# Kernel optimization log

Hardware: AMD Instinct MI355X
Metric: run time of the kernel (lower is better)

Reference implementation:

```python
import jax, jax.numpy as jnp
import numpy as np

B, L, H, I, K, G = 2, 4096, 1024, 2048, 4, 8  # batch, seq, hidden, intermediate, kernel, conv groups
EPS = 1e-5


def setup_inputs() -> dict:
    key = jax.random.key(0)
    ks = jax.random.split(key, 8)
    s = 0.02
    return {
        "hidden_states": jax.random.normal(ks[0], (B, L, H), jnp.float32),
        "in_proj_w": jax.random.normal(ks[1], (2 * I, H), jnp.float32) * s,  # Linear(H -> 2I), no bias
        "conv_w": jax.random.normal(ks[2], (I, I // G, K), jnp.float32) * s,  # grouped Conv1d weight [O, I/G, K]
        "conv_b": jax.random.normal(ks[3], (I,), jnp.float32) * s,
        "ln_g": jnp.ones((I,), jnp.float32),
        "ln_b": jnp.zeros((I,), jnp.float32),
        "fc_w": jax.random.normal(ks[4], (H, I), jnp.float32) * s,   # MLP c_fc: I -> H
        "fc_b": jnp.zeros((H,), jnp.float32),
        "cproj_w": jax.random.normal(ks[5], (I, H), jnp.float32) * s,  # MLP c_proj: H -> I
        "cproj_b": jnp.zeros((I,), jnp.float32),
        "out_w": jax.random.normal(ks[6], (H, I), jnp.float32) * s,  # out_proj: I -> H, no bias
    }


def _layernorm(x, g, b):
    m = x.mean(-1, keepdims=True)
    v = jnp.var(x, axis=-1, keepdims=True)
    return (x - m) * jax.lax.rsqrt(v + EPS) * g + b


def reference(hidden_states, in_proj_w, conv_w, conv_b, ln_g, ln_b, fc_w, fc_b, cproj_w, cproj_b, out_w):
    # in_proj then chunk into hidden / gate (torch chunks along channel dim after transpose)
    p = hidden_states @ in_proj_w.T              # [B, L, 2I]
    h, gate = p[..., :I], p[..., I:]             # [B, L, I] each
    gate = jax.nn.silu(gate)
    # causal grouped conv1d: ConstantPad1d((K-1, 0)) + Conv1d(groups=G)
    hc = jnp.transpose(h, (0, 2, 1))             # [B, I, L]
    conv = jax.lax.conv_general_dilated(
        hc, conv_w, window_strides=(1,), padding=[(K - 1, 0)],
        feature_group_count=G, dimension_numbers=("NCH", "OIH", "NCH"))
    conv = conv + conv_b[None, :, None]          # [B, I, L]
    h = jnp.transpose(conv, (0, 2, 1)) * gate    # gated mixing, [B, L, I]
    residual = h
    hn = _layernorm(h, ln_g, ln_b)
    # MLP (dropout is identity at inference): I -> H -> silu -> I
    m = jax.nn.silu(hn @ fc_w.T + fc_b) @ cproj_w.T + cproj_b
    h = m + residual
    return h @ out_w.T                           # [B, L, H]
```

## Files before the change

kernel.cpp:

```cpp
#include <hip/hip_runtime.h>
#include <stdint.h>


#define TOKENS 8192
#define HDIM   1024
#define IDIM   2048
#define PADL   4099

typedef __bf16 bf16_t;
typedef __bf16 bf16x8 __attribute__((ext_vector_type(8)));
typedef __bf16 bf16x4 __attribute__((ext_vector_type(4)));
typedef float  f32x4  __attribute__((ext_vector_type(4)));

__device__ __forceinline__ float silu_f(float v) { return v / (1.f + __expf(-v)); }

__global__ __launch_bounds__(256) void cvt_f32_bf16(const float* __restrict__ in,
                                                    bf16_t* __restrict__ out, int n4) {
  int i = blockIdx.x * 256 + threadIdx.x;
  if (i < n4) {
    float4 v = reinterpret_cast<const float4*>(in)[i];
    bf16x4 o = {(bf16_t)v.x, (bf16_t)v.y, (bf16_t)v.z, (bf16_t)v.w};
    reinterpret_cast<bf16x4*>(out)[i] = o;
  }
}

__global__ __launch_bounds__(256) void cvt_weights(
    const float* __restrict__ ipf, const float* __restrict__ fcf,
    const float* __restrict__ cpf, const float* __restrict__ outf,
    bf16_t* __restrict__ ipb, bf16_t* __restrict__ fcb,
    bf16_t* __restrict__ cpb, bf16_t* __restrict__ outb) {
  int i = blockIdx.x * 256 + threadIdx.x;
  const float* src; bf16_t* dst; int off;
  if (i < 1048576)      { src = ipf;  dst = ipb;  off = i; }
  else if (i < 1572864) { src = fcf;  dst = fcb;  off = i - 1048576; }
  else if (i < 2097152) { src = cpf;  dst = cpb;  off = i - 1572864; }
  else                  { src = outf; dst = outb; off = i - 2097152; }
  float4 v = reinterpret_cast<const float4*>(src)[off];
  bf16x4 o = {(bf16_t)v.x, (bf16_t)v.y, (bf16_t)v.z, (bf16_t)v.w};
  reinterpret_cast<bf16x4*>(dst)[off] = o;
}

__global__ __launch_bounds__(256) void expand_convw(const float* __restrict__ cw,
                                                    bf16_t* __restrict__ w2) {
  int idx = blockIdx.x * 256 + threadIdx.x;
  int o = idx >> 10, r = idx & 1023, k = r >> 8, ci = r & 255;
  w2[idx] = (bf16_t)cw[(o << 10) + (ci << 2) + k];
}

__global__ __launch_bounds__(256) void zero_pad_rows(bf16_t* __restrict__ hpad) {
  int idx = blockIdx.x * 256 + threadIdx.x;
  if (idx < 2 * 3 * IDIM) {
    int b = idx / (3 * IDIM);
    int r = idx - b * (3 * IDIM);
    hpad[(size_t)b * PADL * IDIM + r] = (bf16_t)0.f;
  }
}

__global__ __launch_bounds__(256) void ln_k(const bf16_t* __restrict__ x,
                                            const float* __restrict__ g,
                                            const float* __restrict__ b,
                                            bf16_t* __restrict__ out) {
  int row = blockIdx.x, tid = threadIdx.x;
  const bf16_t* xr = x + (size_t)row * IDIM;
  bf16x8 v = *reinterpret_cast<const bf16x8*>(xr + tid * 8);
  float f[8], s = 0.f, ss = 0.f;
#pragma unroll
  for (int j = 0; j < 8; ++j) { f[j] = (float)v[j]; s += f[j]; ss += f[j] * f[j]; }
#pragma unroll
  for (int o = 32; o; o >>= 1) { s += __shfl_xor(s, o); ss += __shfl_xor(ss, o); }
  __shared__ float red[2][4];
  int wv = tid >> 6, lane = tid & 63;
  if (lane == 0) { red[0][wv] = s; red[1][wv] = ss; }
  __syncthreads();
  s  = red[0][0] + red[0][1] + red[0][2] + red[0][3];
  ss = red[1][0] + red[1][1] + red[1][2] + red[1][3];
  float mean = s * (1.f / IDIM);
  float var  = ss * (1.f / IDIM) - mean * mean;
  float rstd = rsqrtf(var + 1e-5f);
  bf16x8 o8;
#pragma unroll
  for (int j = 0; j < 8; ++j) {
    int c = tid * 8 + j;
    o8[j] = (bf16_t)((f[j] - mean) * rstd * g[c] + b[c]);
  }
  *reinterpret_cast<bf16x8*>(out + (size_t)row * IDIM + tid * 8) = o8;
}

#define BARR __builtin_amdgcn_s_barrier()

template <int KIND, int N, int K, int BM, int BN, int WM, int WN>
__global__ __launch_bounds__(WM * WN * 64, 2) void gemm_k(
    const bf16_t* __restrict__ A, const bf16_t* __restrict__ W,
    const float* __restrict__ bias, const bf16_t* __restrict__ extra,
    void* __restrict__ outp, bf16_t* __restrict__ hpad_out,
    bf16_t* __restrict__ gate_out) {
  constexpr int NWAVE = WM * WN;
  constexpr int TM = BM / WM, TN = BN / WN;
  constexpr int MR = TM / 16, NR = TN / 16;
  constexpr int NT = K / 64;
  constexpr int NTN = N / BN;
  constexpr int SA = BM / (NWAVE * 8);
  constexpr int SB = BN / (NWAVE * 8);
  __shared__ bf16_t As[2][BM][64];
  __shared__ bf16_t Bs[2][BN][64];
  const int tid = threadIdx.x, lane = tid & 63, wid = tid >> 6;
  const int wr = wid / WN, wc = wid % WN;
  int bid = blockIdx.x;
  { const int cpx = gridDim.x >> 3; bid = (bid & 7) * cpx + (bid >> 3); }
  const int t0 = (bid / NTN) * BM, n0 = (bid % NTN) * BN;

  const int sw16 = (((lane & 7) ^ (lane >> 3)) << 4);

  int cur = 0;

  auto stageA = [&](int j, int tt) {
    const int row = j * NWAVE * 8 + wid * 8 + (lane >> 3);
    char* dst = (char*)&As[tt & 1][0][0] + row * 128 + ((lane & 7) << 4);
    const char* src;
    if constexpr (KIND == 1) {
      const int grow = t0 + row, b = grow >> 12, pos = grow & 4095;
      src = (const char*)A +
            (((size_t)b * PADL + pos + (tt >> 2)) * IDIM + (n0 & ~255) + ((tt & 3) << 6)) * 2 + sw16;
    } else {
      src = (const char*)A + ((size_t)(t0 + row) * K + tt * 64) * 2 + sw16;
    }
    __builtin_amdgcn_global_load_lds((const __attribute__((address_space(1))) void*)src,
                                     (__attribute__((address_space(3))) void*)dst, 16, 0, 0);
  };
  auto stageB = [&](int j, int tt) {
    const int row = j * NWAVE * 8 + wid * 8 + (lane >> 3);
    char* dst = (char*)&Bs[tt & 1][0][0] + row * 128 + ((lane & 7) << 4);
    const char* src = (const char*)W + ((size_t)(n0 + row) * K + tt * 64) * 2 + sw16;
    __builtin_amdgcn_global_load_lds((const __attribute__((address_space(1))) void*)src,
                                     (__attribute__((address_space(3))) void*)dst, 16, 0, 0);
  };
  auto stageAll = [&](int tt) {
#pragma unroll
    for (int j = 0; j < SA; ++j) stageA(j, tt);
#pragma unroll
    for (int j = 0; j < SB; ++j) stageB(j, tt);
  };
  auto readA = [&](int mi, int s) -> bf16x8 {
    const int row = wr * TM + mi * 16 + (lane & 15);
    const int cb = (s * 64 + ((lane >> 4) << 4)) ^ ((lane & 7) << 4);
    return *(const bf16x8*)((const char*)&As[cur][0][0] + row * 128 + cb);
  };
  auto readB = [&](int ni, int s) -> bf16x8 {
    const int row = wc * TN + ni * 16 + (lane & 15);
    const int cb = (s * 64 + ((lane >> 4) << 4)) ^ ((lane & 7) << 4);
    return *(const bf16x8*)((const char*)&Bs[cur][0][0] + row * 128 + cb);
  };

  f32x4 acc[MR][NR] = {};
  bf16x8 aF[MR / 2][2], bF[NR][2];

#define MMA_QUAD(MH, NH)                                                        \
  _Pragma("unroll") for (int mi = 0; mi < MR / 2; ++mi) {                       \
    _Pragma("unroll") for (int ni = 0; ni < NR / 2; ++ni) {                     \
      _Pragma("unroll") for (int s = 0; s < 2; ++s) {                           \
        acc[(MH) * (MR / 2) + mi][(NH) * (NR / 2) + ni] =                       \
            __builtin_amdgcn_mfma_f32_16x16x32_bf16(                            \
                aF[mi][s], bF[(NH) * (NR / 2) + ni][s],                         \
                acc[(MH) * (MR / 2) + mi][(NH) * (NR / 2) + ni], 0, 0, 0);      \
      }                                                                         \
    }                                                                           \
  }

  stageAll(0);
  asm volatile("s_waitcnt vmcnt(0)");
  BARR;

  for (int t = 0; t < NT; ++t) {
    cur = t & 1;
    const bool nx = (t + 1) < NT;
#pragma unroll
    for (int mi = 0; mi < MR / 2; ++mi)
#pragma unroll
      for (int s = 0; s < 2; ++s) aF[mi][s] = readA(mi, s);
#pragma unroll
    for (int ni = 0; ni < NR / 2; ++ni)
#pragma unroll
      for (int s = 0; s < 2; ++s) bF[ni][s] = readB(ni, s);
    if (nx) stageAll(t + 1);
    BARR;
    __builtin_amdgcn_s_setprio(1);
    MMA_QUAD(0, 0);
    __builtin_amdgcn_s_setprio(0);
    BARR;
#pragma unroll
    for (int ni = 0; ni < NR / 2; ++ni)
#pragma unroll
      for (int s = 0; s < 2; ++s) bF[NR / 2 + ni][s] = readB(NR / 2 + ni, s);
    BARR;
    __builtin_amdgcn_s_setprio(1);
    MMA_QUAD(0, 1);
    __builtin_amdgcn_s_setprio(0);
    BARR;
#pragma unroll
    for (int mi = 0; mi < MR / 2; ++mi)
#pragma unroll
      for (int s = 0; s < 2; ++s) aF[mi][s] = readA(MR / 2 + mi, s);
    BARR;
    __builtin_amdgcn_s_setprio(1);
    MMA_QUAD(1, 1);
    __builtin_amdgcn_s_setprio(0);
    BARR;
    __builtin_amdgcn_s_setprio(1);
    MMA_QUAD(1, 0);
    __builtin_amdgcn_s_setprio(0);
    if (nx) asm volatile("s_waitcnt vmcnt(0)");
    BARR;
  }
#undef MMA_QUAD

#pragma unroll
  for (int mi = 0; mi < MR; ++mi) {
#pragma unroll
    for (int ni = 0; ni < NR; ++ni) {
      const int col = n0 + wc * TN + ni * 16 + (lane & 15);
      float bv = 0.f;
      if constexpr (KIND == 1 || KIND == 2 || KIND == 3) bv = bias[col];
#pragma unroll
      for (int r = 0; r < 4; ++r) {
        const int row = t0 + wr * TM + mi * 16 + ((lane >> 4) << 2) + r;
        float v = acc[mi][ni][r];
        if constexpr (KIND == 0) {
          if (n0 < IDIM) {
            int b = row >> 12, pos = row & 4095;
            hpad_out[((size_t)b * PADL + 3 + pos) * IDIM + col] = (bf16_t)v;
          } else {
            gate_out[(size_t)row * IDIM + (col - IDIM)] = (bf16_t)silu_f(v);
          }
        } else if constexpr (KIND == 1) {
          float gt = (float)extra[(size_t)row * IDIM + col];
          ((bf16_t*)outp)[(size_t)row * N + col] = (bf16_t)((v + bv) * gt);
        } else if constexpr (KIND == 2) {
          ((bf16_t*)outp)[(size_t)row * N + col] = (bf16_t)silu_f(v + bv);
        } else if constexpr (KIND == 3) {
          float res = (float)extra[(size_t)row * N + col];
          ((bf16_t*)outp)[(size_t)row * N + col] = (bf16_t)(v + bv + res);
        } else {
          ((float*)outp)[(size_t)row * N + col] = v;
        }
      }
    }
  }
}

extern "C" void kernel_launch(void* const* d_in, const int* in_sizes, int n_in,
                              void* d_out, int out_size, void* d_ws, size_t ws_size,
                              hipStream_t stream) {
  const float* hs       = (const float*)d_in[0];
  const float* in_projw = (const float*)d_in[1];
  const float* conv_w   = (const float*)d_in[2];
  const float* conv_b   = (const float*)d_in[3];
  const float* ln_g     = (const float*)d_in[4];
  const float* ln_b     = (const float*)d_in[5];
  const float* fc_w     = (const float*)d_in[6];
  const float* fc_b     = (const float*)d_in[7];
  const float* cproj_w  = (const float*)d_in[8];
  const float* cproj_b  = (const float*)d_in[9];
  const float* out_w    = (const float*)d_in[10];

  char* ws = (char*)d_ws;
  size_t off = 0;
  auto alloc = [&](size_t bytes) {
    char* p = ws + off;
    off += (bytes + 255) & ~(size_t)255;
    return p;
  };
  bf16_t* hs_b  = (bf16_t*)alloc((size_t)TOKENS * HDIM * 2);
  bf16_t* w_ip  = (bf16_t*)alloc((size_t)2 * IDIM * HDIM * 2);
  bf16_t* w2c   = (bf16_t*)alloc((size_t)IDIM * 1024 * 2);
  bf16_t* w_fc  = (bf16_t*)alloc((size_t)HDIM * IDIM * 2);
  bf16_t* w_cp  = (bf16_t*)alloc((size_t)IDIM * HDIM * 2);
  bf16_t* w_out = (bf16_t*)alloc((size_t)HDIM * IDIM * 2);
  bf16_t* hpad  = (bf16_t*)alloc((size_t)2 * PADL * IDIM * 2);
  bf16_t* gate  = (bf16_t*)alloc((size_t)TOKENS * IDIM * 2);
  bf16_t* xres  = (bf16_t*)alloc((size_t)TOKENS * IDIM * 2);

  bf16_t* t_buf = hs_b;
  bf16_t* hn    = gate;
  bf16_t* h2    = hpad;

  cvt_f32_bf16<<<8192, 256, 0, stream>>>(hs, hs_b, TOKENS * HDIM / 4);
  cvt_weights<<<10240, 256, 0, stream>>>(in_projw, fc_w, cproj_w, out_w,
                                         w_ip, w_fc, w_cp, w_out);
  expand_convw<<<8192, 256, 0, stream>>>(conv_w, w2c);
  zero_pad_rows<<<48, 256, 0, stream>>>(hpad);

  gemm_k<0, 4096, 1024, 256, 256, 2, 4><<<512, 512, 0, stream>>>(
      hs_b, w_ip, nullptr, nullptr, nullptr, hpad, gate);
  gemm_k<1, 2048, 1024, 256, 256, 2, 4><<<256, 512, 0, stream>>>(
      hpad, w2c, conv_b, gate, xres, nullptr, nullptr);
  ln_k<<<TOKENS, 256, 0, stream>>>(xres, ln_g, ln_b, hn);
  gemm_k<2, 1024, 2048, 256, 128, 2, 4><<<256, 512, 0, stream>>>(
      hn, w_fc, fc_b, nullptr, t_buf, nullptr, nullptr);
  gemm_k<3, 2048, 1024, 256, 256, 2, 4><<<256, 512, 0, stream>>>(
      t_buf, w_cp, cproj_b, xres, h2, nullptr, nullptr);
  gemm_k<4, 1024, 2048, 256, 128, 2, 4><<<256, 512, 0, stream>>>(
      h2, w_out, nullptr, nullptr, d_out, nullptr, nullptr);
}
```

Measured before the change: 463.4 us.

## Interleave next-tile LDS staging across MMA quadrants with partial vmcnt waits

```diff
diff --git a/kernel.cpp b/kernel.cpp
--- a/kernel.cpp
+++ b/kernel.cpp
@@ -88,6 +88,13 @@
 
 #define BARR __builtin_amdgcn_s_barrier()
 
+template <int N> __device__ __forceinline__ void vwait() {
+  if constexpr (N == 0) asm volatile("s_waitcnt vmcnt(0)");
+  else if constexpr (N == 2) asm volatile("s_waitcnt vmcnt(2)");
+  else if constexpr (N == 3) asm volatile("s_waitcnt vmcnt(3)");
+  else if constexpr (N == 4) asm volatile("s_waitcnt vmcnt(4)");
+}
+
 template <int KIND, int N, int K, int BM, int BN, int WM, int WN>
 __global__ __launch_bounds__(WM * WN * 64, 2) void gemm_k(
     const bf16_t* __restrict__ A, const bf16_t* __restrict__ W,
@@ -101,6 +108,9 @@
   constexpr int NTN = N / BN;
   constexpr int SA = BM / (NWAVE * 8);
   constexpr int SB = BN / (NWAVE * 8);
+  static_assert(TM / SA == WN * 8, "A stage map");
+  static_assert(TN / SB == WM * 8, "B stage map");
+  static_assert(SA == 4 && (SB == 4 || SB == 2), "ledger assumes SA=4");
   __shared__ bf16_t As[2][BM][64];
   __shared__ bf16_t Bs[2][BN][64];
   const int tid = threadIdx.x, lane = tid & 63, wid = tid >> 6;
@@ -114,7 +124,7 @@
   int cur = 0;
 
   auto stageA = [&](int j, int tt) {
-    const int row = j * NWAVE * 8 + wid * 8 + (lane >> 3);
+    const int row = wr * TM + j * (TM / SA) + (wc << 3) + (lane >> 3);
     char* dst = (char*)&As[tt & 1][0][0] + row * 128 + ((lane & 7) << 4);
     const char* src;
     if constexpr (KIND == 1) {
@@ -128,17 +138,11 @@
                                      (__attribute__((address_space(3))) void*)dst, 16, 0, 0);
   };
   auto stageB = [&](int j, int tt) {
-    const int row = j * NWAVE * 8 + wid * 8 + (lane >> 3);
+    const int row = wc * TN + j * (TN / SB) + (wr << 3) + (lane >> 3);
     char* dst = (char*)&Bs[tt & 1][0][0] + row * 128 + ((lane & 7) << 4);
     const char* src = (const char*)W + ((size_t)(n0 + row) * K + tt * 64) * 2 + sw16;
     __builtin_amdgcn_global_load_lds((const __attribute__((address_space(1))) void*)src,
                                      (__attribute__((address_space(3))) void*)dst, 16, 0, 0);
-  };
-  auto stageAll = [&](int tt) {
-#pragma unroll
-    for (int j = 0; j < SA; ++j) stageA(j, tt);
-#pragma unroll
-    for (int j = 0; j < SB; ++j) stageB(j, tt);
   };
   auto readA = [&](int mi, int s) -> bf16x8 {
     const int row = wr * TM + mi * 16 + (lane & 15);
@@ -166,8 +170,10 @@
     }                                                                           \
   }
 
-  stageAll(0);
-  asm volatile("s_waitcnt vmcnt(0)");
+  stageA(0, 0); stageA(1, 0); stageB(0, 0); stageB(1, 0);
+  if constexpr (SB == 4) { stageB(2, 0); stageB(3, 0); }
+  stageA(2, 0); stageA(3, 0);
+  if constexpr (SB == 4) vwait<4>(); else vwait<3>();
   BARR;
 
   for (int t = 0; t < NT; ++t) {
@@ -181,34 +187,45 @@
     for (int ni = 0; ni < NR / 2; ++ni)
 #pragma unroll
       for (int s = 0; s < 2; ++s) bF[ni][s] = readB(ni, s);
-    if (nx) stageAll(t + 1);
+    if (nx) { stageA(0, t + 1); stageA(1, t + 1); }
     BARR;
     __builtin_amdgcn_s_setprio(1);
     MMA_QUAD(0, 0);
     __builtin_amdgcn_s_setprio(0);
+    if (nx) vwait<4>(); else vwait<2>();
     BARR;
 #pragma unroll
     for (int ni = 0; ni < NR / 2; ++ni)
 #pragma unroll
       for (int s = 0; s < 2; ++s) bF[NR / 2 + ni][s] = readB(NR / 2 + ni, s);
+    if (nx) { stageB(0, t + 1); stageB(1, t + 1); }
     BARR;
     __builtin_amdgcn_s_setprio(1);
     MMA_QUAD(0, 1);
     __builtin_amdgcn_s_setprio(0);
+    if (nx) vwait<4>(); else vwait<0>();
     BARR;
 #pragma unroll
     for (int mi = 0; mi < MR / 2; ++mi)
 #pragma unroll
       for (int s = 0; s < 2; ++s) aF[mi][s] = readA(MR / 2 + mi, s);
+    if (nx) {
+      if constexpr (SB == 4) { stageB(2, t + 1); stageB(3, t + 1); }
+      else { stageA(2, t + 1); }
+    }
     BARR;
     __builtin_amdgcn_s_setprio(1);
     MMA_QUAD(1, 1);
     __builtin_amdgcn_s_setprio(0);
     BARR;
+    if (nx) {
+      if constexpr (SB == 4) { stageA(2, t + 1); stageA(3, t + 1); }
+      else { stageA(3, t + 1); }
+    }
     __builtin_amdgcn_s_setprio(1);
     MMA_QUAD(1, 0);
     __builtin_amdgcn_s_setprio(0);
-    if (nx) asm volatile("s_waitcnt vmcnt(0)");
+    if (nx) { if constexpr (SB == 4) vwait<4>(); else vwait<3>(); }
     BARR;
   }
 #undef MMA_QUAD
```

Measured after the change: 410.2 us. 1.13x faster.
